# Performance work log

Measured on AMD Instinct MI355X. Metric: run time of the kernel, lower is better.

## Reference

```python
import jax, jax.numpy as jnp
import numpy as np

N, C, HI, WI = 8, 3, 512, 512   # src_img NCHW (input_img_size)
HO, WO = 2048, 2048             # output canvas (output_img_size[2:])
EPS = 1e-8


def _transform_one(img, coor_row):
    """Replicates: sigmoid box params -> theta -> F.affine_grid -> F.grid_sample
    (bilinear, zeros padding, align_corners=False). Theta has zero off-diagonals,
    so the grid is separable in x/y and the bilinear sample factorizes.
    img: [C, HI, WI]; coor_row: [4]. Returns (sample [C,HO,WO], mask [HO,WO])."""
    x = jax.nn.sigmoid(coor_row[0]) * WO
    y = jax.nn.sigmoid(coor_row[1]) * HO
    w = jax.nn.sigmoid(coor_row[2]) * WO
    h = jax.nn.sigmoid(coor_row[3]) * HO
    a = WO / (w + EPS)
    tx = 2.0 / WO * (WO / 2.0 - x) * a
    b = HO / (h + EPS)
    ty = 2.0 / HO * (HO / 2.0 - y) * b
    # affine_grid base coords (align_corners=False): center-of-pixel normalized
    xs = (2.0 * jnp.arange(WO, dtype=img.dtype) + 1.0) / WO - 1.0
    ys = (2.0 * jnp.arange(HO, dtype=img.dtype) + 1.0) / HO - 1.0
    gx = a * xs + tx          # [WO]
    gy = b * ys + ty          # [HO]
    # grid_sample unnormalize (align_corners=False)
    ix = ((gx + 1.0) * WI - 1.0) / 2.0
    iy = ((gy + 1.0) * HI - 1.0) / 2.0
    x0f = jnp.floor(ix); y0f = jnp.floor(iy)
    wx1 = ix - x0f; wx0 = 1.0 - wx1
    wy1 = iy - y0f; wy0 = 1.0 - wy1
    x0 = x0f.astype(jnp.int32); x1 = x0 + 1
    y0 = y0f.astype(jnp.int32); y1 = y0 + 1
    vx0 = ((x0 >= 0) & (x0 < WI)).astype(img.dtype)
    vx1 = ((x1 >= 0) & (x1 < WI)).astype(img.dtype)
    vy0 = ((y0 >= 0) & (y0 < HI)).astype(img.dtype)
    vy1 = ((y1 >= 0) & (y1 < HI)).astype(img.dtype)
    x0c = jnp.clip(x0, 0, WI - 1); x1c = jnp.clip(x1, 0, WI - 1)
    y0c = jnp.clip(y0, 0, HI - 1); y1c = jnp.clip(y1, 0, HI - 1)
    wyv0 = wy0 * vy0; wyv1 = wy1 * vy1
    wxv0 = wx0 * vx0; wxv1 = wx1 * vx1
    # separable bilinear gather with zero padding
    rows = img[:, y0c, :] * wyv0[None, :, None] + img[:, y1c, :] * wyv1[None, :, None]  # [C,HO,WI]
    samp = rows[:, :, x0c] * wxv0[None, None, :] + rows[:, :, x1c] * wxv1[None, None, :]  # [C,HO,WO]
    # grid_sample of an all-ones mask == sum of in-bounds bilinear weights (separable)
    mask = (wyv0 + wyv1)[:, None] * (wxv0 + wxv1)[None, :]  # [HO,WO]
    return samp, mask


def _composite(src_img, bg_img, coor):
    def step(bg, inp):
        img, c = inp
        s, m = _transform_one(img, c)
        bg = bg * (1.0 - m)[None, None] + (s * m[None])[None]
        return bg, None
    bg, _ = jax.lax.scan(step, bg_img, (src_img, coor))
    return bg


def setup_inputs() -> dict:
    key = jax.random.key(0)
    k1, k2, k3 = jax.random.split(key, 3)
    src_img = jax.random.normal(k1, (N, C, HI, WI), dtype=jnp.float32)
    bg_img = jax.random.uniform(k2, (1, C, HO, WO), dtype=jnp.float32)
    coor = jax.random.normal(k3, (N, 4), dtype=jnp.float32)  # nn.Parameter
    return {"src_img": src_img, "bg_img": bg_img, "coor": coor}


def reference(src_img, bg_img, coor):
    return _composite(src_img, bg_img, coor)
```

## Files before the change

kernel.cpp:

```cpp
#include <hip/hip_runtime.h>

#define WI 512
#define HI 512
#define WO 2048
#define HO 2048
#define NIMG 8
#define CCH 3
#define EPS 1e-8f
#define ROWS 8

__global__ void diffcomp_params(const float* __restrict__ coor,
                                float4* __restrict__ params) {
    int n = threadIdx.x;
    if (n < NIMG) {
        float cx = coor[n * 4 + 0];
        float cy = coor[n * 4 + 1];
        float cw = coor[n * 4 + 2];
        float ch = coor[n * 4 + 3];
        float x = (1.0f / (1.0f + expf(-cx))) * (float)WO;
        float y = (1.0f / (1.0f + expf(-cy))) * (float)HO;
        float w = (1.0f / (1.0f + expf(-cw))) * (float)WO;
        float h = (1.0f / (1.0f + expf(-ch))) * (float)HO;
        float a  = (float)WO / (w + EPS);
        float tx = (2.0f / (float)WO) * ((float)WO * 0.5f - x) * a;
        float b  = (float)HO / (h + EPS);
        float ty = (2.0f / (float)HO) * ((float)HO * 0.5f - y) * b;
        params[n] = make_float4(a, tx, b, ty);
    }
}

__launch_bounds__(256)
__global__ void diffcomp_main(const float* __restrict__ src,
                              const float* __restrict__ bg,
                              const float4* __restrict__ params,
                              float* __restrict__ out) {
    const int wo  = blockIdx.x * 256 + threadIdx.x;
    const int ho0 = blockIdx.y * ROWS;

    float4 P[NIMG];
#pragma unroll
    for (int n = 0; n < NIMG; n++) P[n] = params[n];

    float wxv0[NIMG], wxv1[NIMG], mx[NIMG];
    int   x0c[NIMG], x1c[NIMG];
    const float xs = (2.0f * (float)wo + 1.0f) / (float)WO - 1.0f;
#pragma unroll
    for (int n = 0; n < NIMG; n++) {
        float a  = P[n].x, tx = P[n].y;
        float gx = a * xs + tx;
        float ix = (((gx + 1.0f) * (float)WI) - 1.0f) * 0.5f;
        float x0f = floorf(ix);
        float wx1 = ix - x0f;
        float wx0 = 1.0f - wx1;
        float x1f = x0f + 1.0f;
        float vx0 = (x0f >= 0.0f && x0f < (float)WI) ? 1.0f : 0.0f;
        float vx1 = (x1f >= 0.0f && x1f < (float)WI) ? 1.0f : 0.0f;
        wxv0[n] = wx0 * vx0;
        wxv1[n] = wx1 * vx1;
        x0c[n] = (int)fminf(fmaxf(x0f, 0.0f), (float)(WI - 1));
        x1c[n] = (int)fminf(fmaxf(x1f, 0.0f), (float)(WI - 1));
        mx[n] = wxv0[n] + wxv1[n];
    }

    for (int r = 0; r < ROWS; r++) {
        const int ho = ho0 + r;
        const float ys = (2.0f * (float)ho + 1.0f) / (float)HO - 1.0f;
        const int pix = ho * WO + wo;

        float acc0 = bg[0 * HO * WO + pix];
        float acc1 = bg[1 * HO * WO + pix];
        float acc2 = bg[2 * HO * WO + pix];

#pragma unroll
        for (int n = 0; n < NIMG; n++) {
            float b  = P[n].z, ty = P[n].w;
            float gy = b * ys + ty;
            float iy = (((gy + 1.0f) * (float)HI) - 1.0f) * 0.5f;
            float y0f = floorf(iy);
            float wy1 = iy - y0f;
            float wy0 = 1.0f - wy1;
            float y1f = y0f + 1.0f;
            float vy0 = (y0f >= 0.0f && y0f < (float)HI) ? 1.0f : 0.0f;
            float vy1 = (y1f >= 0.0f && y1f < (float)HI) ? 1.0f : 0.0f;
            float wyv0 = wy0 * vy0;
            float wyv1 = wy1 * vy1;
            float my = wyv0 + wyv1;
            float m  = my * mx[n];
            if (m > 0.0f) {
                int y0i = (int)fminf(fmaxf(y0f, 0.0f), (float)(HI - 1));
                int y1i = (int)fminf(fmaxf(y1f, 0.0f), (float)(HI - 1));
                const float* ib = src + n * (CCH * HI * WI);
                const int o00 = y0i * WI + x0c[n];
                const int o01 = y0i * WI + x1c[n];
                const int o10 = y1i * WI + x0c[n];
                const int o11 = y1i * WI + x1c[n];
                const float om = 1.0f - m;
                float s0, s1, s2;
                {
                    const float* p = ib + 0 * HI * WI;
                    float v00 = p[o00], v01 = p[o01], v10 = p[o10], v11 = p[o11];
                    s0 = (v00 * wyv0 + v10 * wyv1) * wxv0[n]
                       + (v01 * wyv0 + v11 * wyv1) * wxv1[n];
                }
                {
                    const float* p = ib + 1 * HI * WI;
                    float v00 = p[o00], v01 = p[o01], v10 = p[o10], v11 = p[o11];
                    s1 = (v00 * wyv0 + v10 * wyv1) * wxv0[n]
                       + (v01 * wyv0 + v11 * wyv1) * wxv1[n];
                }
                {
                    const float* p = ib + 2 * HI * WI;
                    float v00 = p[o00], v01 = p[o01], v10 = p[o10], v11 = p[o11];
                    s2 = (v00 * wyv0 + v10 * wyv1) * wxv0[n]
                       + (v01 * wyv0 + v11 * wyv1) * wxv1[n];
                }
                acc0 = acc0 * om + s0 * m;
                acc1 = acc1 * om + s1 * m;
                acc2 = acc2 * om + s2 * m;
            }
        }

        out[0 * HO * WO + pix] = acc0;
        out[1 * HO * WO + pix] = acc1;
        out[2 * HO * WO + pix] = acc2;
    }
}

extern "C" void kernel_launch(void* const* d_in, const int* in_sizes, int n_in,
                              void* d_out, int out_size, void* d_ws, size_t ws_size,
                              hipStream_t stream) {
    const float* src  = (const float*)d_in[0];
    const float* bg   = (const float*)d_in[1];
    const float* coor = (const float*)d_in[2];
    float* out = (float*)d_out;
    float4* params = (float4*)d_ws;

    hipLaunchKernelGGL(diffcomp_params, dim3(1), dim3(64), 0, stream, coor, params);
    dim3 grid(WO / 256, HO / ROWS);
    hipLaunchKernelGGL(diffcomp_main, grid, dim3(256), 0, stream,
                       src, bg, params, out);
}
```

Baseline: 154.9 us.

## Precompute per-image x/y bilinear tables and read them in the main kernel

After: 162.2 us. 4.7% more time.

```diff
diff --git a/kernel.cpp b/kernel.cpp
--- a/kernel.cpp
+++ b/kernel.cpp
@@ -7,7 +7,143 @@
 #define NIMG 8
 #define CCH 3
 #define EPS 1e-8f
-#define ROWS 8
+#define ROWS 4
+
+__global__ void diffcomp_tables(const float* __restrict__ coor,
+                                int4* __restrict__ xtab,
+                                int4* __restrict__ ytab) {
+    const int idx = blockIdx.x * 256 + threadIdx.x;
+    const bool isY = idx >= NIMG * WO;
+    const int rem = isY ? idx - NIMG * WO : idx;
+    const int n   = rem >> 11;
+    const int pos = rem & 2047;
+
+    const float cx = coor[n * 4 + 0];
+    const float cy = coor[n * 4 + 1];
+    const float cw = coor[n * 4 + 2];
+    const float ch = coor[n * 4 + 3];
+
+    float a, t, INF;
+    if (!isY) {
+        const float x = (1.0f / (1.0f + expf(-cx))) * (float)WO;
+        const float w = (1.0f / (1.0f + expf(-cw))) * (float)WO;
+        a = (float)WO / (w + EPS);
+        t = (2.0f / (float)WO) * ((float)WO * 0.5f - x) * a;
+        INF = (float)WI;
+    } else {
+        const float y = (1.0f / (1.0f + expf(-cy))) * (float)HO;
+        const float h = (1.0f / (1.0f + expf(-ch))) * (float)HO;
+        a = (float)HO / (h + EPS);
+        t = (2.0f / (float)HO) * ((float)HO * 0.5f - y) * a;
+        INF = (float)HI;
+    }
+
+    const float s  = (2.0f * (float)pos + 1.0f) / 2048.0f - 1.0f;
+    const float g  = a * s + t;
+    const float ic = ((g + 1.0f) * INF - 1.0f) * 0.5f;
+    const float f0 = floorf(ic);
+    const float fr1 = ic - f0;
+    const float fr0 = 1.0f - fr1;
+    const float f1 = f0 + 1.0f;
+    const float v0 = (f0 >= 0.0f && f0 < INF) ? 1.0f : 0.0f;
+    const float v1 = (f1 >= 0.0f && f1 < INF) ? 1.0f : 0.0f;
+    const float w0 = fr0 * v0;
+    const float w1 = fr1 * v1;
+    int c0 = (int)fminf(fmaxf(f0, 0.0f), INF - 1.0f);
+    int c1 = (int)fminf(fmaxf(f1, 0.0f), INF - 1.0f);
+    if (isY) { c0 *= WI; c1 *= WI; }
+
+    int4 e;
+    e.x = __float_as_int(w0);
+    e.y = __float_as_int(w1);
+    e.z = c0;
+    e.w = c1;
+    (isY ? ytab : xtab)[(n << 11) + pos] = e;
+}
+
+__launch_bounds__(256)
+__global__ void diffcomp_main2(const float* __restrict__ src,
+                               const float* __restrict__ bg,
+                               const int4* __restrict__ xtab,
+                               const int4* __restrict__ ytab,
+                               float* __restrict__ out) {
+    __shared__ int4 ylds[ROWS * NIMG];
+
+    const int tid = threadIdx.x;
+    const int wo  = blockIdx.x * 256 + tid;
+    const int ho0 = blockIdx.y * ROWS;
+
+    if (tid < ROWS * NIMG) {
+        const int r = tid >> 3;
+        const int n = tid & 7;
+        ylds[tid] = ytab[(n << 11) + ho0 + r];
+    }
+
+    float wx0[NIMG], wx1[NIMG], mxv[NIMG];
+    int   ox0[NIMG], ox1[NIMG];
+#pragma unroll
+    for (int n = 0; n < NIMG; n++) {
+        const int4 e = xtab[(n << 11) + wo];
+        wx0[n] = __int_as_float(e.x);
+        wx1[n] = __int_as_float(e.y);
+        ox0[n] = e.z;
+        ox1[n] = e.w;
+        mxv[n] = wx0[n] + wx1[n];
+    }
+
+    __syncthreads();
+
+    for (int r = 0; r < ROWS; r++) {
+        const int ho  = ho0 + r;
+        const int pix = ho * WO + wo;
+
+        float acc0 = bg[0 * HO * WO + pix];
+        float acc1 = bg[1 * HO * WO + pix];
+        float acc2 = bg[2 * HO * WO + pix];
+
+#pragma unroll
+        for (int n = 0; n < NIMG; n++) {
+            const int4 ey = ylds[r * NIMG + n];
+            const float wy0 = __int_as_float(ey.x);
+            const float wy1 = __int_as_float(ey.y);
+            const float m = (wy0 + wy1) * mxv[n];
+            if (m > 0.0f) {
+                const float* ib = src + n * (CCH * HI * WI);
+                const int o00 = ey.z + ox0[n];
+                const int o01 = ey.z + ox1[n];
+                const int o10 = ey.w + ox0[n];
+                const int o11 = ey.w + ox1[n];
+                const float om = 1.0f - m;
+                float s0, s1, s2;
+                {
+                    const float* p = ib + 0 * HI * WI;
+                    const float v00 = p[o00], v01 = p[o01], v10 = p[o10], v11 = p[o11];
+                    s0 = (v00 * wy0 + v10 * wy1) * wx0[n]
+                       + (v01 * wy0 + v11 * wy1) * wx1[n];
+                }
+                {
+                    const float* p = ib + 1 * HI * WI;
+                    const float v00 = p[o00], v01 = p[o01], v10 = p[o10], v11 = p[o11];
+                    s1 = (v00 * wy0 + v10 * wy1) * wx0[n]
+                       + (v01 * wy0 + v11 * wy1) * wx1[n];
+                }
+                {
+                    const float* p = ib + 2 * HI * WI;
+                    const float v00 = p[o00], v01 = p[o01], v10 = p[o10], v11 = p[o11];
+                    s2 = (v00 * wy0 + v10 * wy1) * wx0[n]
+                       + (v01 * wy0 + v11 * wy1) * wx1[n];
+                }
+                acc0 = acc0 * om + s0 * m;
+                acc1 = acc1 * om + s1 * m;
+                acc2 = acc2 * om + s2 * m;
+            }
+        }
+
+        out[0 * HO * WO + pix] = acc0;
+        out[1 * HO * WO + pix] = acc1;
+        out[2 * HO * WO + pix] = acc2;
+    }
+}
 
 __global__ void diffcomp_params(const float* __restrict__ coor,
                                 float4* __restrict__ params) {
@@ -35,7 +171,7 @@
                               const float4* __restrict__ params,
                               float* __restrict__ out) {
     const int wo  = blockIdx.x * 256 + threadIdx.x;
-    const int ho0 = blockIdx.y * ROWS;
+    const int ho0 = blockIdx.y * 8;
 
     float4 P[NIMG];
 #pragma unroll
@@ -62,7 +198,7 @@
         mx[n] = wxv0[n] + wxv1[n];
     }
 
-    for (int r = 0; r < ROWS; r++) {
+    for (int r = 0; r < 8; r++) {
         const int ho = ho0 + r;
         const float ys = (2.0f * (float)ho + 1.0f) / (float)HO - 1.0f;
         const int pix = ho * WO + wo;
@@ -84,8 +220,7 @@
             float vy1 = (y1f >= 0.0f && y1f < (float)HI) ? 1.0f : 0.0f;
             float wyv0 = wy0 * vy0;
             float wyv1 = wy1 * vy1;
-            float my = wyv0 + wyv1;
-            float m  = my * mx[n];
+            float m = (wyv0 + wyv1) * mx[n];
             if (m > 0.0f) {
                 int y0i = (int)fminf(fmaxf(y0f, 0.0f), (float)(HI - 1));
                 int y1i = (int)fminf(fmaxf(y1f, 0.0f), (float)(HI - 1));
@@ -133,10 +268,22 @@
     const float* bg   = (const float*)d_in[1];
     const float* coor = (const float*)d_in[2];
     float* out = (float*)d_out;
-    float4* params = (float4*)d_ws;
-
-    hipLaunchKernelGGL(diffcomp_params, dim3(1), dim3(64), 0, stream, coor, params);
-    dim3 grid(WO / 256, HO / ROWS);
-    hipLaunchKernelGGL(diffcomp_main, grid, dim3(256), 0, stream,
-                       src, bg, params, out);
-}
+
+    const size_t tab_bytes = (size_t)2 * NIMG * 2048 * sizeof(int4);
+
+    if (ws_size >= tab_bytes) {
+        int4* xtab = (int4*)d_ws;
+        int4* ytab = xtab + NIMG * 2048;
+        hipLaunchKernelGGL(diffcomp_tables, dim3(128), dim3(256), 0, stream,
+                           coor, xtab, ytab);
+        dim3 grid(WO / 256, HO / ROWS);
+        hipLaunchKernelGGL(diffcomp_main2, grid, dim3(256), 0, stream,
+                           src, bg, xtab, ytab, out);
+    } else {
+        float4* params = (float4*)d_ws;
+        hipLaunchKernelGGL(diffcomp_params, dim3(1), dim3(64), 0, stream, coor, params);
+        dim3 grid(WO / 256, HO / 8);
+        hipLaunchKernelGGL(diffcomp_main, grid, dim3(256), 0, stream,
+                           src, bg, params, out);
+    }
+}
```

## Stage interleaved source rows in LDS and process one output row per block

Applied to the files above, without the earlier changes.

Result: slower. 172.9 us (+11.6%).

```diff
diff --git a/kernel.cpp b/kernel.cpp
--- a/kernel.cpp
+++ b/kernel.cpp
@@ -7,7 +7,7 @@
 #define NIMG 8
 #define CCH 3
 #define EPS 1e-8f
-#define ROWS 8
+#define PLANE (HI * WI)
 
 __global__ void diffcomp_params(const float* __restrict__ coor,
                                 float4* __restrict__ params) {
@@ -30,12 +30,167 @@
 }
 
 __launch_bounds__(256)
+__global__ void diffcomp_interleave(const float* __restrict__ src,
+                                    float4* __restrict__ srcI) {
+    const int idx = blockIdx.x * 256 + threadIdx.x;
+    const int n   = idx >> 18;
+    const int rem = idx & (PLANE - 1);
+    const float* p = src + n * (CCH * PLANE) + rem;
+    float4 v;
+    v.x = p[0 * PLANE];
+    v.y = p[1 * PLANE];
+    v.z = p[2 * PLANE];
+    v.w = 0.0f;
+    srcI[idx] = v;
+}
+
+__launch_bounds__(256)
+__global__ void diffcomp_main5(const float4* __restrict__ srcI,
+                               const float* __restrict__ bg,
+                               const float4* __restrict__ params,
+                               float* __restrict__ out) {
+    __shared__ float4 rows[2][2][WI];
+
+    const int tid = threadIdx.x;
+    const int ho  = blockIdx.x;
+    const float ys = (2.0f * (float)ho + 1.0f) / (float)HO - 1.0f;
+
+    float4 P[NIMG];
+#pragma unroll
+    for (int n = 0; n < NIMG; n++) P[n] = params[n];
+
+    unsigned cov = 0u;
+#pragma unroll
+    for (int n = 0; n < NIMG; n++) {
+        const float gy  = P[n].z * ys + P[n].w;
+        const float iy  = ((gy + 1.0f) * (float)HI - 1.0f) * 0.5f;
+        const float y0f = floorf(iy);
+        const float fy1 = iy - y0f;
+        const float fy0 = 1.0f - fy1;
+        const float y1f = y0f + 1.0f;
+        const float v0  = (y0f >= 0.0f && y0f < (float)HI) ? 1.0f : 0.0f;
+        const float v1  = (y1f >= 0.0f && y1f < (float)HI) ? 1.0f : 0.0f;
+        const float my  = fy0 * v0 + fy1 * v1;
+        if (my > 0.0f) cov |= (1u << n);
+    }
+
+    float acc[CCH][8];
+#pragma unroll
+    for (int c = 0; c < CCH; c++)
+#pragma unroll
+        for (int p = 0; p < 8; p++)
+            acc[c][p] = bg[c * HO * WO + ho * WO + p * 256 + tid];
+
+    while (cov) {
+        int ns[2];
+        int cnt = 1;
+        ns[0] = (int)__builtin_ctz(cov); cov &= cov - 1u;
+        if (cov) { ns[1] = (int)__builtin_ctz(cov); cov &= cov - 1u; cnt = 2; }
+
+        __syncthreads();
+
+        for (int s = 0; s < cnt; s++) {
+            const int n = ns[s];
+            const float gy  = P[n].z * ys + P[n].w;
+            const float iy  = ((gy + 1.0f) * (float)HI - 1.0f) * 0.5f;
+            const float y0f = floorf(iy);
+            const float y1f = y0f + 1.0f;
+            const int y0o = ((int)fminf(fmaxf(y0f, 0.0f), (float)(HI - 1))) << 9;
+            const int y1o = ((int)fminf(fmaxf(y1f, 0.0f), (float)(HI - 1))) << 9;
+            const float4* ip = srcI + (n << 18);
+#pragma unroll
+            for (int j = 0; j < 2; j++) {
+                const int idx = j * 256 + tid;
+                rows[s][0][idx] = ip[y0o + idx];
+                rows[s][1][idx] = ip[y1o + idx];
+            }
+        }
+        __syncthreads();
+
+        for (int s = 0; s < cnt; s++) {
+            const int n = ns[s];
+            const float gy  = P[n].z * ys + P[n].w;
+            const float iy  = ((gy + 1.0f) * (float)HI - 1.0f) * 0.5f;
+            const float y0f = floorf(iy);
+            const float fy1 = iy - y0f;
+            const float fy0 = 1.0f - fy1;
+            const float y1f = y0f + 1.0f;
+            const float v0  = (y0f >= 0.0f && y0f < (float)HI) ? 1.0f : 0.0f;
+            const float v1  = (y1f >= 0.0f && y1f < (float)HI) ? 1.0f : 0.0f;
+            const float w0  = fy0 * v0;
+            const float w1  = fy1 * v1;
+#pragma unroll
+            for (int j = 0; j < 2; j++) {
+                const int idx = j * 256 + tid;
+                const float4 r0 = rows[s][0][idx];
+                const float4 r1 = rows[s][1][idx];
+                float4 rc;
+                rc.x = r0.x * w0 + r1.x * w1;
+                rc.y = r0.y * w0 + r1.y * w1;
+                rc.z = r0.z * w0 + r1.z * w1;
+                rc.w = 0.0f;
+                rows[s][0][idx] = rc;
+            }
+        }
+        __syncthreads();
+
+        for (int s = 0; s < cnt; s++) {
+            const int n = ns[s];
+            const float gy  = P[n].z * ys + P[n].w;
+            const float iy  = ((gy + 1.0f) * (float)HI - 1.0f) * 0.5f;
+            const float y0f = floorf(iy);
+            const float fy1 = iy - y0f;
+            const float fy0 = 1.0f - fy1;
+            const float y1f = y0f + 1.0f;
+            const float v0y = (y0f >= 0.0f && y0f < (float)HI) ? 1.0f : 0.0f;
+            const float v1y = (y1f >= 0.0f && y1f < (float)HI) ? 1.0f : 0.0f;
+            const float my  = fy0 * v0y + fy1 * v1y;
+            const float a   = P[n].x;
+            const float tx  = P[n].y;
+#pragma unroll
+            for (int p = 0; p < 8; p++) {
+                const int wo = p * 256 + tid;
+                const float xs  = (2.0f * (float)wo + 1.0f) / (float)WO - 1.0f;
+                const float gx  = a * xs + tx;
+                const float ix  = ((gx + 1.0f) * (float)WI - 1.0f) * 0.5f;
+                const float x0f = floorf(ix);
+                const float fx1 = ix - x0f;
+                const float fx0 = 1.0f - fx1;
+                const float x1f = x0f + 1.0f;
+                const float v0  = (x0f >= 0.0f && x0f < (float)WI) ? 1.0f : 0.0f;
+                const float v1  = (x1f >= 0.0f && x1f < (float)WI) ? 1.0f : 0.0f;
+                const float wx0 = fx0 * v0;
+                const float wx1 = fx1 * v1;
+                const int x0c = (int)fminf(fmaxf(x0f, 0.0f), (float)(WI - 1));
+                const int x1c = (int)fminf(fmaxf(x1f, 0.0f), (float)(WI - 1));
+                const float4 t0 = rows[s][0][x0c];
+                const float4 t1 = rows[s][0][x1c];
+                const float m  = my * (wx0 + wx1);
+                const float om = 1.0f - m;
+                const float s0 = t0.x * wx0 + t1.x * wx1;
+                const float s1 = t0.y * wx0 + t1.y * wx1;
+                const float s2 = t0.z * wx0 + t1.z * wx1;
+                acc[0][p] = acc[0][p] * om + s0 * m;
+                acc[1][p] = acc[1][p] * om + s1 * m;
+                acc[2][p] = acc[2][p] * om + s2 * m;
+            }
+        }
+    }
+
+#pragma unroll
+    for (int c = 0; c < CCH; c++)
+#pragma unroll
+        for (int p = 0; p < 8; p++)
+            out[c * HO * WO + ho * WO + p * 256 + tid] = acc[c][p];
+}
+
+__launch_bounds__(256)
 __global__ void diffcomp_main(const float* __restrict__ src,
                               const float* __restrict__ bg,
                               const float4* __restrict__ params,
                               float* __restrict__ out) {
     const int wo  = blockIdx.x * 256 + threadIdx.x;
-    const int ho0 = blockIdx.y * ROWS;
+    const int ho0 = blockIdx.y * 8;
 
     float4 P[NIMG];
 #pragma unroll
@@ -62,9 +217,9 @@
         mx[n] = wxv0[n] + wxv1[n];
     }
 
-    for (int r = 0; r < ROWS; r++) {
+    for (int r = 0; r < 8; r++) {
         const int ho = ho0 + r;
-        const float ys = (2.0f * (float)ho + 1.0f) / (float)HO - 1.0f;
+        const float ysr = (2.0f * (float)ho + 1.0f) / (float)HO - 1.0f;
         const int pix = ho * WO + wo;
 
         float acc0 = bg[0 * HO * WO + pix];
@@ -74,49 +229,37 @@
 #pragma unroll
         for (int n = 0; n < NIMG; n++) {
             float b  = P[n].z, ty = P[n].w;
-            float gy = b * ys + ty;
+            float gy = b * ysr + ty;
             float iy = (((gy + 1.0f) * (float)HI) - 1.0f) * 0.5f;
             float y0f = floorf(iy);
             float wy1 = iy - y0f;
             float wy0 = 1.0f - wy1;
-            float y1f = y0f + 1.0f;
-            float vy0 = (y0f >= 0.0f && y0f < (float)HI) ? 1.0f : 0.0f;
-            float vy1 = (y1f >= 0.0f && y1f < (float)HI) ? 1.0f : 0.0f;
-            float wyv0 = wy0 * vy0;
-            float wyv1 = wy1 * vy1;
-            float my = wyv0 + wyv1;
-            float m  = my * mx[n];
+        float y1f = y0f + 1.0f;
+        float vy0 = (y0f >= 0.0f && y0f < (float)HI) ? 1.0f : 0.0f;
+        float vy1 = (y1f >= 0.0f && y1f < (float)HI) ? 1.0f : 0.0f;
+        float wyv0 = wy0 * vy0;
+        float wyv1 = wy1 * vy1;
+        float m = (wyv0 + wyv1) * mx[n];
             if (m > 0.0f) {
                 int y0i = (int)fminf(fmaxf(y0f, 0.0f), (float)(HI - 1));
                 int y1i = (int)fminf(fmaxf(y1f, 0.0f), (float)(HI - 1));
-                const float* ib = src + n * (CCH * HI * WI);
+                const float* ib = src + n * (CCH * PLANE);
                 const int o00 = y0i * WI + x0c[n];
                 const int o01 = y0i * WI + x1c[n];
                 const int o10 = y1i * WI + x0c[n];
                 const int o11 = y1i * WI + x1c[n];
                 const float om = 1.0f - m;
-                float s0, s1, s2;
-                {
-                    const float* p = ib + 0 * HI * WI;
-                    float v00 = p[o00], v01 = p[o01], v10 = p[o10], v11 = p[o11];
-                    s0 = (v00 * wyv0 + v10 * wyv1) * wxv0[n]
-                       + (v01 * wyv0 + v11 * wyv1) * wxv1[n];
+                float sc[CCH];
+#pragma unroll
+                for (int c = 0; c < CCH; c++) {
+                    const float* p = ib + c * PLANE;
+                    const float v00 = p[o00], v01 = p[o01], v10 = p[o10], v11 = p[o11];
+                    sc[c] = (v00 * wyv0 + v10 * wyv1) * wxv0[n]
+                          + (v01 * wyv0 + v11 * wyv1) * wxv1[n];
                 }
-                {
-                    const float* p = ib + 1 * HI * WI;
-                    float v00 = p[o00], v01 = p[o01], v10 = p[o10], v11 = p[o11];
-                    s1 = (v00 * wyv0 + v10 * wyv1) * wxv0[n]
-                       + (v01 * wyv0 + v11 * wyv1) * wxv1[n];
-                }
-                {
-                    const float* p = ib + 2 * HI * WI;
-                    float v00 = p[o00], v01 = p[o01], v10 = p[o10], v11 = p[o11];
-                    s2 = (v00 * wyv0 + v10 * wyv1) * wxv0[n]
-                       + (v01 * wyv0 + v11 * wyv1) * wxv1[n];
-                }
-                acc0 = acc0 * om + s0 * m;
-                acc1 = acc1 * om + s1 * m;
-                acc2 = acc2 * om + s2 * m;
+                acc0 = acc0 * om + sc[0] * m;
+                acc1 = acc1 * om + sc[1] * m;
+                acc2 = acc2 * om + sc[2] * m;
             }
         }
 
@@ -133,10 +276,22 @@
     const float* bg   = (const float*)d_in[1];
     const float* coor = (const float*)d_in[2];
     float* out = (float*)d_out;
+
+    const size_t par_bytes  = NIMG * sizeof(float4);
+    const size_t srcI_bytes = (size_t)NIMG * PLANE * sizeof(float4);
+
     float4* params = (float4*)d_ws;
-
     hipLaunchKernelGGL(diffcomp_params, dim3(1), dim3(64), 0, stream, coor, params);
-    dim3 grid(WO / 256, HO / ROWS);
-    hipLaunchKernelGGL(diffcomp_main, grid, dim3(256), 0, stream,
-                       src, bg, params, out);
-}
+
+    if (ws_size >= par_bytes + srcI_bytes + 256) {
+        float4* srcI = (float4*)((char*)d_ws + 256);
+        hipLaunchKernelGGL(diffcomp_interleave, dim3(NIMG * PLANE / 256), dim3(256),
+                           0, stream, src, srcI);
+        hipLaunchKernelGGL(diffcomp_main5, dim3(HO), dim3(256), 0, stream,
+                           srcI, bg, params, out);
+    } else {
+        dim3 grid(WO / 256, HO / 8);
+        hipLaunchKernelGGL(diffcomp_main, grid, dim3(256), 0, stream,
+                           src, bg, params, out);
+    }
+}
```
